# Kernel optimization log

Measured on AMD Instinct MI355X. Metric: run time of the kernel, lower is better.

## Reference

```python
import jax, jax.numpy as jnp
import numpy as np

B, S, D, H = 8, 512, 1024, 16
HD = D // H                      # head_dim = 64
MAX_SEQ_LEN = 512
SCRATCH_SLOTS = 64


def _rope_cache():
    inv_freq = 1.0 / (10000.0 ** (jnp.arange(0, HD, 2, dtype=jnp.float32) / HD))
    t = jnp.arange(MAX_SEQ_LEN + SCRATCH_SLOTS, dtype=jnp.float32)
    freqs = jnp.outer(t, inv_freq)               # [T, HD//2]
    freqs = jnp.concatenate([freqs, freqs], -1)  # [T, HD]
    return jnp.sin(freqs), jnp.cos(freqs)


def rotate_half(x):
    x1, x2 = x[..., : x.shape[-1] // 2], x[..., x.shape[-1] // 2 :]
    return jnp.concatenate([-x2, x1], axis=-1)


def setup_inputs() -> dict:
    key = jax.random.key(0)
    ks = jax.random.split(key, 5)
    def w(k):
        return jax.random.normal(k, (D, D), dtype=jnp.float32) * 0.02
    return {
        "x": jax.random.normal(ks[0], (B, S, D), dtype=jnp.float32),
        "Wq": w(ks[1]), "bq": jnp.zeros((D,), jnp.float32),
        "Wk": w(ks[2]), "bk": jnp.zeros((D,), jnp.float32),
        "Wv": w(ks[3]), "bv": jnp.zeros((D,), jnp.float32),
        "Wo": w(ks[4]), "bo": jnp.zeros((D,), jnp.float32),
    }


def reference(x, Wq, bq, Wk, bk, Wv, bv, Wo, bo):
    b, s, d = x.shape
    sin_c, cos_c = _rope_cache()
    scale = jnp.array(HD ** (-0.5), dtype=jnp.float32)

    xh = x.astype(jnp.float16)
    def lin(inp, W, bias):  # nnx.Linear with dtype=fp16: cast params + input to fp16
        return inp @ W.astype(jnp.float16) + bias.astype(jnp.float16)

    q = lin(xh, Wq, bq).reshape(b, s, H, HD)
    k = lin(xh, Wk, bk).reshape(b, s, H, HD)
    v = lin(xh, Wv, bv).reshape(b, s, H, HD)

    sin = sin_c[:s, None, :].astype(jnp.float32)  # [s,1,HD]
    cos = cos_c[:s, None, :].astype(jnp.float32)
    qf = q.astype(jnp.float32)
    kf = k.astype(jnp.float32)
    q = qf * cos + rotate_half(qf) * sin
    k = kf * cos + rotate_half(kf) * sin
    v = v.astype(jnp.float32)
    q = q * scale  # module's explicit scale

    # [b,H,s,HD]
    q, k, v = (t.transpose(0, 2, 1, 3) for t in (q, k, v))

    # jax.nn.dot_product_attention additionally scales by 1/sqrt(HD)
    logits = jnp.einsum("bhqd,bhkd->bhqk", q, k) * scale
    probs = jax.nn.softmax(logits, axis=-1)
    out = jnp.einsum("bhqk,bhkd->bhqd", probs, v)
    out = out.transpose(0, 2, 1, 3).reshape(b, s, d)
    return lin(out.astype(jnp.float16), Wo, bo)
```

## Files before the change

kernel.cpp:

```cpp
#include <hip/hip_runtime.h>

typedef _Float16 half8 __attribute__((ext_vector_type(8)));
typedef _Float16 half4v __attribute__((ext_vector_type(4)));
typedef float f32x4 __attribute__((ext_vector_type(4)));

#define OFF_CS    0u
#define OFF_XH    (1u<<20)
#define OFF_WQKVT (OFF_XH + 8u*1024u*1024u)
#define OFF_WOT   (OFF_WQKVT + 8u*1024u*1024u)
#define OFF_QKV   (OFF_WOT + 2u*1024u*1024u)
#define OFF_ATTN  OFF_WQKVT


__device__ __forceinline__ void gload16(const _Float16* g, _Float16* l) {
  __builtin_amdgcn_global_load_lds((const __attribute__((address_space(1))) void*)g,
                                   (__attribute__((address_space(3))) void*)l, 16, 0, 0);
}

__global__ void prep_k(const float* __restrict__ x,
                       const float* __restrict__ W0, const float* __restrict__ W1,
                       const float* __restrict__ W2, const float* __restrict__ W3,
                       _Float16* __restrict__ xh, _Float16* __restrict__ wqkvt,
                       _Float16* __restrict__ wot, float2* __restrict__ cs) {
  int bid = blockIdx.x, tid = threadIdx.x;
  if (bid < 4096) {
    int i = bid * 256 + tid;
    float4 v = ((const float4*)x)[i];
    half4v h;
    h[0] = (_Float16)v.x; h[1] = (_Float16)v.y; h[2] = (_Float16)v.z; h[3] = (_Float16)v.w;
    *(half4v*)(xh + (size_t)i * 4) = h;
  } else if (bid < 8192) {
    __shared__ float tile[32][33];
    int tb = bid - 4096;
    int z = tb >> 10, t = tb & 1023, by = t >> 5, bx = t & 31;
    const float* W = z == 0 ? W0 : z == 1 ? W1 : z == 2 ? W2 : W3;
    _Float16* Wt = z < 3 ? wqkvt + (size_t)z * 1048576 : wot;
    int r = tid >> 3, c0 = (tid & 7) * 4;
    float4 v = *(const float4*)(W + (size_t)(by * 32 + r) * 1024 + bx * 32 + c0);
    tile[r][c0] = v.x; tile[r][c0 + 1] = v.y; tile[r][c0 + 2] = v.z; tile[r][c0 + 3] = v.w;
    __syncthreads();
    half4v h;
#pragma unroll
    for (int j = 0; j < 4; j++) h[j] = (_Float16)tile[c0 + j][r];
    *(half4v*)(Wt + (size_t)(bx * 32 + r) * 1024 + by * 32 + c0) = h;
  } else {
    int idx = (bid - 8192) * 256 + tid;
    int pos = idx >> 5, j = idx & 31;
    float inv = powf(10000.0f, -(float)j * (1.0f / 32.0f));
    float f = (float)pos * inv;
    cs[idx] = make_float2(cosf(f), sinf(f));
  }
}

template <int MODE>
__global__ __launch_bounds__(256, MODE == 0 ? 3 : 2) void gemm_k(
    const _Float16* __restrict__ A, const _Float16* __restrict__ Bt,
    const float* __restrict__ b0, const float* __restrict__ b1, const float* __restrict__ b2,
    void* __restrict__ Cv, const float2* __restrict__ cs) {
  constexpr int BM  = (MODE == 0) ? 128 : 64;
  constexpr int N   = (MODE == 0) ? 3072 : 1024;
  constexpr int NBX = N / 128;
  constexpr int MF  = BM / 32;
  constexpr int ACH = BM / 64;
  __shared__ _Float16 Ar[3][BM * 32];
  __shared__ _Float16 Br[3][128 * 32];

  int nwg = gridDim.x, cpx = nwg >> 3;
  int bid = blockIdx.x;
  int wgid = (bid & 7) * cpx + (bid >> 3);
  int by = wgid / NBX, bx = wgid % NBX;

  int tid = threadIdx.x, lane = tid & 63, w = tid >> 6;
  int wr = w >> 1, wc = w & 1;
  int arow = lane & 15, ag = lane >> 4;
  int s8 = (((arow & 1) << 2) | ag) ^ ((arow >> 1) & 7);

  int qq = (lane & 7) ^ (lane >> 3);
  int rloc = ((lane >> 3) << 1) + (qq >> 2);
  int gcol = (qq & 3) * 8;

  const _Float16* Ag = A + (size_t)(by * BM) * 1024;
  const _Float16* Bg = Bt + (size_t)(bx * 128) * 1024;

  f32x4 acc[MF][4] = {};

  auto stage = [&](int t) {
    int slot = t % 3;
    int k0 = t * 32;
#pragma unroll
    for (int i = 0; i < ACH; i++) {
      int c = w * ACH + i;
      gload16(Ag + (size_t)(c * 16 + rloc) * 1024 + k0 + gcol, &Ar[slot][c * 512]);
    }
#pragma unroll
    for (int i = 0; i < 2; i++) {
      int c = w * 2 + i;
      gload16(Bg + (size_t)(c * 16 + rloc) * 1024 + k0 + gcol, &Br[slot][c * 512]);
    }
  };

  stage(0); stage(1);
  if (MODE == 0) asm volatile("s_waitcnt vmcnt(4)" ::: "memory");
  else           asm volatile("s_waitcnt vmcnt(3)" ::: "memory");
  __builtin_amdgcn_s_barrier();
  __builtin_amdgcn_sched_barrier(0);

  for (int t = 0; t < 32; ++t) {
    if (t < 30) stage(t + 2);
    __builtin_amdgcn_sched_barrier(0);
    const _Float16* Ac = &Ar[t % 3][0];
    const _Float16* Bc = &Br[t % 3][0];
    half8 a[MF], b[4];
#pragma unroll
    for (int m = 0; m < MF; m++) {
      int R = wr * (BM / 2) + m * 16 + arow;
      a[m] = *(const half8*)&Ac[(R >> 1) * 64 + s8 * 8];
    }
#pragma unroll
    for (int n = 0; n < 4; n++) {
      int R = wc * 64 + n * 16 + arow;
      b[n] = *(const half8*)&Bc[(R >> 1) * 64 + s8 * 8];
    }
    __builtin_amdgcn_s_setprio(1);
#pragma unroll
    for (int m = 0; m < MF; m++)
#pragma unroll
      for (int n = 0; n < 4; n++)
        acc[m][n] = __builtin_amdgcn_mfma_f32_16x16x32_f16(a[m], b[n], acc[m][n], 0, 0, 0);
    __builtin_amdgcn_s_setprio(0);
    __builtin_amdgcn_sched_barrier(0);
    if (t < 30) {
      if (MODE == 0) asm volatile("s_waitcnt vmcnt(4)" ::: "memory");
      else           asm volatile("s_waitcnt vmcnt(3)" ::: "memory");
    } else if (t == 30) {
      asm volatile("s_waitcnt vmcnt(0)" ::: "memory");
    }
    if (t < 31) {
      __builtin_amdgcn_s_barrier();
      __builtin_amdgcn_sched_barrier(0);
    }
  }

  int gc0 = bx * 128 + wc * 64;
  if (MODE == 0) {
    const float* bp = gc0 < 1024 ? b0 : (gc0 < 2048 ? b1 : b2);
    float bb_[4];
#pragma unroll
    for (int n = 0; n < 4; n++) bb_[n] = bp[(gc0 & 1023) + n * 16 + arow];
    _Float16* C = (_Float16*)Cv;
    if (gc0 < 2048) {
      bool isQ = gc0 < 1024;
#pragma unroll
      for (int m = 0; m < MF; m++) {
        int gr = by * BM + wr * (BM / 2) + m * 16 + ag * 4;
#pragma unroll
        for (int r = 0; r < 4; r++) {
          int row = gr + r, pos = row & 511;
#pragma unroll
          for (int n = 0; n < 2; n++) {
            int j = n * 16 + arow;
            float av = (float)(_Float16)(acc[m][n][r] + bb_[n]);
            float bv = (float)(_Float16)(acc[m][n + 2][r] + bb_[n + 2]);
            float2 tt = cs[pos * 32 + j];
            float o0 = av * tt.x - bv * tt.y;
            float o1 = bv * tt.x + av * tt.y;
            if (isQ) { o0 *= 0.015625f; o1 *= 0.015625f; }
            C[(size_t)row * 3072 + gc0 + j]      = (_Float16)o0;
            C[(size_t)row * 3072 + gc0 + j + 32] = (_Float16)o1;
          }
        }
      }
    } else {
#pragma unroll
      for (int m = 0; m < MF; m++) {
        int gr = by * BM + wr * (BM / 2) + m * 16 + ag * 4;
        int bb2 = gr >> 9;
        int st6 = (gr & 511) >> 6;
        int s63 = gr & 63;
#pragma unroll
        for (int n = 0; n < 4; n++) {
          int colh = gc0 - 2048 + n * 16 + arow;
          int h = colh >> 6, hd = colh & 63;
          half4v v4;
#pragma unroll
          for (int r = 0; r < 4; r++) v4[r] = (_Float16)(acc[m][n][r] + bb_[n]);
          size_t addr = ((size_t)(bb2 * 512 + hd * 8 + st6)) * 3072 + 2048 + h * 64 + s63;
          *(half4v*)(C + addr) = v4;
        }
      }
    }
  } else {
    float* C = (float*)Cv;
#pragma unroll
    for (int m = 0; m < MF; m++) {
      int gr = by * BM + wr * (BM / 2) + m * 16 + ag * 4;
#pragma unroll
      for (int n = 0; n < 4; n++) {
        int gc = gc0 + n * 16 + arow;
        float bb = b0[gc];
#pragma unroll
        for (int r = 0; r < 4; r++)
          C[(size_t)(gr + r) * 1024 + gc] = (float)(_Float16)(acc[m][n][r] + bb);
      }
    }
  }
}

__global__ __launch_bounds__(256, 4) void attn_k(const _Float16* __restrict__ qkv,
                                                 _Float16* __restrict__ out) {
  int id = blockIdx.x;
  int bh = id & 127, qt = id >> 7;
  int b = bh >> 4, h = bh & 15;
  int tid = threadIdx.x, lane = tid & 63, w = tid >> 6;
  int arow = lane & 15, ag = lane >> 4;

  __shared__ _Float16 Ks[64 * 64];
  __shared__ _Float16 Vs[64 * 64];
  __shared__ _Float16 Pl[4][16][72];

  int qrow0 = b * 512 + qt * 64 + w * 16;
  const _Float16* Qp = qkv + (size_t)qrow0 * 3072 + h * 64;
  half8 qa[2];
#pragma unroll
  for (int ks = 0; ks < 2; ks++)
    qa[ks] = *(const half8*)(Qp + (size_t)arow * 3072 + ks * 32 + ag * 8);

  const _Float16* Kb = qkv + (size_t)(b * 512) * 3072 + 1024 + h * 64;

  int srow = lane >> 3;
  int sslot = (lane & 7) ^ srow;
  const _Float16* Ksrc0 = Kb + (size_t)(w * 16 + srow) * 3072 + sslot * 8;
  const _Float16* Vsrc0 = qkv + ((size_t)(b * 512) + (w * 16 + srow) * 8) * 3072
                          + 2048 + h * 64 + sslot * 8;

  int rs = arow & 7;

  float psl[4] = {0.f, 0.f, 0.f, 0.f};
  f32x4 oacc[4] = {};

  for (int st = 0; st < 8; ++st) {
#pragma unroll
    for (int i = 0; i < 2; i++) {
      gload16(Ksrc0 + (size_t)(st * 64 + i * 8) * 3072, &Ks[(w * 16 + i * 8) * 64]);
      gload16(Vsrc0 + (size_t)(i * 64 + st) * 3072,     &Vs[(w * 16 + i * 8) * 64]);
    }
    __syncthreads();

    f32x4 lg[4];
#pragma unroll
    for (int c = 0; c < 4; c++) {
      f32x4 a0 = {};
#pragma unroll
      for (int ks = 0; ks < 2; ks++) {
        int slot = (ks * 4 + ag) ^ rs;
        half8 kb = *(const half8*)&Ks[(c * 16 + arow) * 64 + slot * 8];
        a0 = __builtin_amdgcn_mfma_f32_16x16x32_f16(qa[ks], kb, a0, 0, 0, 0);
      }
      lg[c] = a0;
    }
    _Float16 ph[4][4];
#pragma unroll
    for (int r = 0; r < 4; r++) {
#pragma unroll
      for (int c = 0; c < 4; c++) {
        float p = __builtin_amdgcn_exp2f(lg[c][r] * 1.44269504f);
        psl[r] += p;
        ph[c][r] = (_Float16)p;
      }
    }
#pragma unroll
    for (int c = 0; c < 4; c++)
#pragma unroll
      for (int r = 0; r < 4; r++) Pl[w][ag * 4 + r][c * 16 + arow] = ph[c][r];
#pragma unroll
    for (int ks = 0; ks < 2; ks++) {
      half8 pa = *(const half8*)&Pl[w][arow][ks * 32 + ag * 8];
#pragma unroll
      for (int c = 0; c < 4; c++) {
        int slot = (ks * 4 + ag) ^ rs;
        half8 vb = *(const half8*)&Vs[(c * 16 + arow) * 64 + slot * 8];
        oacc[c] = __builtin_amdgcn_mfma_f32_16x16x32_f16(pa, vb, oacc[c], 0, 0, 0);
      }
    }
    __syncthreads();
  }
#pragma unroll
  for (int r = 0; r < 4; r++)
#pragma unroll
    for (int d = 1; d < 16; d <<= 1) psl[r] += __shfl_xor(psl[r], d, 16);
#pragma unroll
  for (int c = 0; c < 4; c++)
#pragma unroll
    for (int r = 0; r < 4; r++) {
      float v = oacc[c][r] / psl[r];
      out[(size_t)(qrow0 + ag * 4 + r) * 1024 + h * 64 + c * 16 + arow] = (_Float16)v;
    }
}

extern "C" void kernel_launch(void* const* d_in, const int* in_sizes, int n_in,
                              void* d_out, int out_size, void* d_ws, size_t ws_size,
                              hipStream_t stream) {
  const float* x  = (const float*)d_in[0];
  const float* Wq = (const float*)d_in[1];
  const float* bq = (const float*)d_in[2];
  const float* Wk = (const float*)d_in[3];
  const float* bk = (const float*)d_in[4];
  const float* Wv = (const float*)d_in[5];
  const float* bv = (const float*)d_in[6];
  const float* Wo = (const float*)d_in[7];
  const float* bo = (const float*)d_in[8];

  char* ws = (char*)d_ws;
  float2* cs      = (float2*)(ws + OFF_CS);
  _Float16* xh    = (_Float16*)(ws + OFF_XH);
  _Float16* wqkvt = (_Float16*)(ws + OFF_WQKVT);
  _Float16* wot   = (_Float16*)(ws + OFF_WOT);
  _Float16* qkv   = (_Float16*)(ws + OFF_QKV);
  _Float16* attn  = (_Float16*)(ws + OFF_ATTN);

  prep_k<<<8256, 256, 0, stream>>>(x, Wq, Wk, Wv, Wo, xh, wqkvt, wot, cs);
  gemm_k<0><<<768, 256, 0, stream>>>(xh, wqkvt, bq, bk, bv, qkv, cs);
  attn_k<<<1024, 256, 0, stream>>>(qkv, attn);
  gemm_k<1><<<512, 256, 0, stream>>>(attn, wot, bo, bo, bo, d_out, cs);
}
```

Baseline: 90.79 us.

## Process 32 query rows per wave in attention to reuse K/V tiles

Each attention block now covers 128 query rows (32 per wave, as two 16-row groups), so every K/V tile staged in LDS feeds twice as many MFMAs. The grid is halved and launch bounds relaxed to allow more registers per thread. This cuts repeated K/V global loads and barrier overhead per query, but costs more registers, a larger P scratch buffer and fewer blocks in flight.

```diff
diff --git a/kernel.cpp b/kernel.cpp
--- a/kernel.cpp
+++ b/kernel.cpp
@@ -206,7 +206,7 @@
   }
 }
 
-__global__ __launch_bounds__(256, 4) void attn_k(const _Float16* __restrict__ qkv,
+__global__ __launch_bounds__(256, 2) void attn_k(const _Float16* __restrict__ qkv,
                                                  _Float16* __restrict__ out) {
   int id = blockIdx.x;
   int bh = id & 127, qt = id >> 7;
@@ -216,14 +216,16 @@
 
   __shared__ _Float16 Ks[64 * 64];
   __shared__ _Float16 Vs[64 * 64];
-  __shared__ _Float16 Pl[4][16][72];
-
-  int qrow0 = b * 512 + qt * 64 + w * 16;
+  __shared__ _Float16 Pl[4][32][72];
+
+  int qrow0 = b * 512 + qt * 128 + w * 32;
   const _Float16* Qp = qkv + (size_t)qrow0 * 3072 + h * 64;
-  half8 qa[2];
-#pragma unroll
-  for (int ks = 0; ks < 2; ks++)
-    qa[ks] = *(const half8*)(Qp + (size_t)arow * 3072 + ks * 32 + ag * 8);
+  half8 qa[2][2];
+#pragma unroll
+  for (int g = 0; g < 2; g++)
+#pragma unroll
+    for (int ks = 0; ks < 2; ks++)
+      qa[g][ks] = *(const half8*)(Qp + (size_t)(g * 16 + arow) * 3072 + ks * 32 + ag * 8);
 
   const _Float16* Kb = qkv + (size_t)(b * 512) * 3072 + 1024 + h * 64;
 
@@ -235,8 +237,8 @@
 
   int rs = arow & 7;
 
-  float psl[4] = {0.f, 0.f, 0.f, 0.f};
-  f32x4 oacc[4] = {};
+  float psl[2][4] = {};
+  f32x4 oacc[2][4] = {};
 
   for (int st = 0; st < 8; ++st) {
 #pragma unroll
@@ -246,55 +248,67 @@
     }
     __syncthreads();
 
-    f32x4 lg[4];
+    f32x4 lg[2][4];
 #pragma unroll
     for (int c = 0; c < 4; c++) {
-      f32x4 a0 = {};
+      f32x4 a0 = {}, a1 = {};
 #pragma unroll
       for (int ks = 0; ks < 2; ks++) {
         int slot = (ks * 4 + ag) ^ rs;
         half8 kb = *(const half8*)&Ks[(c * 16 + arow) * 64 + slot * 8];
-        a0 = __builtin_amdgcn_mfma_f32_16x16x32_f16(qa[ks], kb, a0, 0, 0, 0);
-      }
-      lg[c] = a0;
-    }
-    _Float16 ph[4][4];
-#pragma unroll
-    for (int r = 0; r < 4; r++) {
-#pragma unroll
-      for (int c = 0; c < 4; c++) {
-        float p = __builtin_amdgcn_exp2f(lg[c][r] * 1.44269504f);
-        psl[r] += p;
-        ph[c][r] = (_Float16)p;
-      }
-    }
-#pragma unroll
-    for (int c = 0; c < 4; c++)
-#pragma unroll
-      for (int r = 0; r < 4; r++) Pl[w][ag * 4 + r][c * 16 + arow] = ph[c][r];
+        a0 = __builtin_amdgcn_mfma_f32_16x16x32_f16(qa[0][ks], kb, a0, 0, 0, 0);
+        a1 = __builtin_amdgcn_mfma_f32_16x16x32_f16(qa[1][ks], kb, a1, 0, 0, 0);
+      }
+      lg[0][c] = a0;
+      lg[1][c] = a1;
+    }
+#pragma unroll
+    for (int g = 0; g < 2; g++) {
+      _Float16 ph[4][4];
+#pragma unroll
+      for (int r = 0; r < 4; r++)
+#pragma unroll
+        for (int c = 0; c < 4; c++) {
+          float p = __builtin_amdgcn_exp2f(lg[g][c][r] * 1.44269504f);
+          psl[g][r] += p;
+          ph[c][r] = (_Float16)p;
+        }
+#pragma unroll
+      for (int c = 0; c < 4; c++)
+#pragma unroll
+        for (int r = 0; r < 4; r++)
+          Pl[w][g * 16 + ag * 4 + r][c * 16 + arow] = ph[c][r];
+    }
 #pragma unroll
     for (int ks = 0; ks < 2; ks++) {
-      half8 pa = *(const half8*)&Pl[w][arow][ks * 32 + ag * 8];
+      half8 pa0 = *(const half8*)&Pl[w][arow][ks * 32 + ag * 8];
+      half8 pa1 = *(const half8*)&Pl[w][16 + arow][ks * 32 + ag * 8];
 #pragma unroll
       for (int c = 0; c < 4; c++) {
         int slot = (ks * 4 + ag) ^ rs;
         half8 vb = *(const half8*)&Vs[(c * 16 + arow) * 64 + slot * 8];
-        oacc[c] = __builtin_amdgcn_mfma_f32_16x16x32_f16(pa, vb, oacc[c], 0, 0, 0);
+        oacc[0][c] = __builtin_amdgcn_mfma_f32_16x16x32_f16(pa0, vb, oacc[0][c], 0, 0, 0);
+        oacc[1][c] = __builtin_amdgcn_mfma_f32_16x16x32_f16(pa1, vb, oacc[1][c], 0, 0, 0);
       }
     }
     __syncthreads();
   }
 #pragma unroll
-  for (int r = 0; r < 4; r++)
-#pragma unroll
-    for (int d = 1; d < 16; d <<= 1) psl[r] += __shfl_xor(psl[r], d, 16);
-#pragma unroll
-  for (int c = 0; c < 4; c++)
-#pragma unroll
-    for (int r = 0; r < 4; r++) {
-      float v = oacc[c][r] / psl[r];
-      out[(size_t)(qrow0 + ag * 4 + r) * 1024 + h * 64 + c * 16 + arow] = (_Float16)v;
-    }
+  for (int g = 0; g < 2; g++)
+#pragma unroll
+    for (int r = 0; r < 4; r++)
+#pragma unroll
+      for (int d = 1; d < 16; d <<= 1) psl[g][r] += __shfl_xor(psl[g][r], d, 16);
+#pragma unroll
+  for (int g = 0; g < 2; g++)
+#pragma unroll
+    for (int c = 0; c < 4; c++)
+#pragma unroll
+      for (int r = 0; r < 4; r++) {
+        float v = oacc[g][c][r] / psl[g][r];
+        out[(size_t)(qrow0 + g * 16 + ag * 4 + r) * 1024 + h * 64 + c * 16 + arow] =
+            (_Float16)v;
+      }
 }
 
 extern "C" void kernel_launch(void* const* d_in, const int* in_sizes, int n_in,
@@ -320,6 +334,6 @@
 
   prep_k<<<8256, 256, 0, stream>>>(x, Wq, Wk, Wv, Wo, xh, wqkvt, wot, cs);
   gemm_k<0><<<768, 256, 0, stream>>>(xh, wqkvt, bq, bk, bv, qkv, cs);
-  attn_k<<<1024, 256, 0, stream>>>(qkv, attn);
+  attn_k<<<512, 256, 0, stream>>>(qkv, attn);
   gemm_k<1><<<512, 256, 0, stream>>>(attn, wot, bo, bo, bo, d_out, cs);
 }
```

New measurement: 89.34 us (median of 2 runs). About the same (-1.6%).
